# Optimization experiments

Hardware: AMD Instinct MI355X
Metric: run time of the kernel (lower is better)

The kernel has to match this reference:

```python
import math
import jax, jax.numpy as jnp
import numpy as np

B, N, C = 64, 1024, 128
RATIO = 0.5
EDGE_P = 0.02  # sparsity of the random binary adjacency


def setup_inputs() -> dict:
    key = jax.random.key(0)
    kx, ka, kw = jax.random.split(key, 3)
    x = jax.random.normal(kx, (B, N, C), dtype=jnp.float32)
    # binary adjacency (realistic graph input); module symmetrizes + clips anyway
    adj = (jax.random.uniform(ka, (B, N, N)) < EDGE_P).astype(jnp.float32)
    # TopKPooling learnable score weight (PyG initializes uniform; normal is fine for a baseline)
    w = jax.random.normal(kw, (C,), dtype=jnp.float32)
    return {"x": x, "adj": adj, "w": w}


def reference(x, adj, w):
    # x: [B, N, C], adj: [B, N, N], w: [C]
    b, n, c = x.shape
    k = int(math.ceil(RATIO * n))  # same k for every graph -> fully batched

    # per-sample: adj_tmp = adj + adj.T; adj_tmp[adj_tmp > 1] = 1
    a = adj + jnp.swapaxes(adj, 1, 2)
    a = jnp.minimum(a, 1.0)

    # TopKPooling score: tanh((x . w) / ||w||), select top-k nodes per graph
    score = jnp.tanh(jnp.einsum("bnc,c->bn", x, w) / jnp.linalg.norm(w))
    top_scores, perm = jax.lax.top_k(score, k)          # [B, k] each, descending

    # gated node features: x[perm] * score[perm]
    x_pool = jnp.take_along_axis(x, perm[..., None], axis=1) * top_scores[..., None]  # [B,k,C]

    # pooled dense adjacency: edges among selected nodes (to_dense_adj counts edges,
    # so entries are 1 where a nonzero edge existed) + 1 on diagonal from add_self_loops
    a_rows = jnp.take_along_axis(a, perm[:, :, None], axis=1)        # [B, k, N]
    a_sub = jnp.take_along_axis(a_rows, perm[:, None, :], axis=2)    # [B, k, k]
    adj_pooled = (a_sub != 0).astype(x.dtype) + jnp.eye(k, dtype=x.dtype)[None]

    return x_pool, adj_pooled
```

## Files before the change

kernel.cpp:

```cpp
#include <hip/hip_runtime.h>
#include <math.h>

#define NB 64
#define NN 1024
#define NC 128
#define NK 512

__global__ __launch_bounds__(1024) void score_kernel(
    const float* __restrict__ x, const float* __restrict__ w,
    double* __restrict__ sacc)
{
    const int i = blockIdx.x;
    const int b = i >> 3, oct = i & 7;
    const int t = threadIdx.x;
    const int c0 = (t & 15) * 8;
    const float4 wa = *(const float4*)(w + c0);
    const float4 wb = *(const float4*)(w + c0 + 4);
    #pragma unroll
    for (int pass = 0; pass < 2; ++pass) {
        int row = oct * 128 + pass * 64 + (t >> 4);
        const float* xr = x + ((size_t)b * NN + row) * NC + c0;
        float4 a  = *(const float4*)xr;
        float4 bb = *(const float4*)(xr + 4);
        double acc = (double)a.x * wa.x + (double)a.y * wa.y
                   + (double)a.z * wa.z + (double)a.w * wa.w
                   + (double)bb.x * wb.x + (double)bb.y * wb.y
                   + (double)bb.z * wb.z + (double)bb.w * wb.w;
        acc += __shfl_xor(acc, 1, 64);
        acc += __shfl_xor(acc, 2, 64);
        acc += __shfl_xor(acc, 4, 64);
        acc += __shfl_xor(acc, 8, 64);
        if ((t & 15) == 0) sacc[(size_t)b * NN + row] = acc;
    }
}

__global__ __launch_bounds__(1024) void rank_xpool_kernel(
    const double* __restrict__ sacc, const float* __restrict__ x,
    const float* __restrict__ w, int* __restrict__ perm,
    float* __restrict__ gate, int* __restrict__ inv,
    float* __restrict__ x_pool)
{
    __shared__ __align__(16) unsigned long long keys[NN];
    __shared__ int rp[1024];
    __shared__ double s_rnw;
    __shared__ int sel_nr[128];
    __shared__ float sel_g[128];
    __shared__ int scount;
    const int i = blockIdx.x;
    const int b = (i & 7) + ((i >> 6) << 3);
    const int h = (i >> 3) & 7;
    const int t = threadIdx.x;

    {
        double sv = sacc[(size_t)b * NN + t];
        long long bits = __double_as_longlong(sv);
        unsigned long long mono =
            (unsigned long long)(bits ^ ((bits >> 63) | 0x8000000000000000LL));
        keys[t] = (mono & ~1023ULL) | (unsigned long long)(1023 - t);
    }
    if (t < 64) {
        double p = (double)w[t] * (double)w[t]
                 + (double)w[t + 64] * (double)w[t + 64];
        #pragma unroll
        for (int off = 32; off > 0; off >>= 1)
            p += __shfl_xor(p, off, 64);
        if (t == 0) s_rnw = 1.0 / sqrt(p);
    }
    if (t == 0) scount = 0;
    __syncthreads();

    const int n  = h * 128 + (t & 127);
    const int jc = t >> 7;
    const unsigned long long mykey = keys[n];
    int r = 0;
    #pragma unroll 8
    for (int j2 = 0; j2 < 64; ++j2) {
        ulonglong2 kk = *(const ulonglong2*)&keys[jc * 128 + j2 * 2];
        r += (kk.x > mykey);
        r += (kk.y > mykey);
    }
    rp[t] = r;
    __syncthreads();
    if (t < 128) {
        int rr = 0;
        #pragma unroll
        for (int c = 0; c < 8; ++c) rr += rp[c * 128 + t];
        int n2 = h * 128 + t;
        inv[b * NN + n2] = (rr < NK) ? rr : -1;
        if (rr < NK) {
            double sv = sacc[(size_t)b * NN + n2];
            float gv = (float)tanh(sv * s_rnw);
            perm[b * NK + rr] = n2;
            gate[b * NK + rr] = gv;
            int slot = atomicAdd(&scount, 1);
            sel_nr[slot] = (n2 << 16) | rr;
            sel_g[slot]  = gv;
        }
    }
    __syncthreads();

    const int cnt = scount;
    const int rowSlot = t >> 5;
    const int lane = t & 31;
    for (int base = 0; base < cnt; base += 32) {
        int idx = base + rowSlot;
        if (idx < cnt) {
            int nr = sel_nr[idx];
            int n2 = nr >> 16, rr = nr & 0xffff;
            float g = sel_g[idx];
            float4 v = *(const float4*)(x + ((size_t)b * NN + n2) * NC + lane * 4);
            v.x *= g; v.y *= g; v.z *= g; v.w *= g;
            *(float4*)(x_pool + ((size_t)b * NK + rr) * NC + lane * 4) = v;
        }
    }
}

__global__ __launch_bounds__(1024) void adj_scan_kernel(
    const float* __restrict__ adj, const int* __restrict__ perm,
    const int* __restrict__ inv, unsigned* __restrict__ bm)
{
    __shared__ unsigned bits[64 * 17];
    __shared__ int sinv[NN];
    const int b = blockIdx.x >> 3;
    const int chunk = blockIdx.x & 7;
    const int t = threadIdx.x;
    for (int idx = t; idx < 64 * 17; idx += 1024) bits[idx] = 0;
    for (int idx = t; idx < NN; idx += 1024) sinv[idx] = inv[b * NN + idx];
    __syncthreads();

    const float* ab = adj + (size_t)b * NN * NN;
    const int* permb = perm + b * NK + chunk * 64;
    const int g  = t >> 8;
    const int lt = t & 255;

    int il = g;
    float4 v0 = *(const float4*)(ab + (size_t)permb[il]      * NN + lt * 4);
    float4 v1 = *(const float4*)(ab + (size_t)permb[il + 4]  * NN + lt * 4);
    float4 v2 = *(const float4*)(ab + (size_t)permb[il + 8]  * NN + lt * 4);
    float4 v3 = *(const float4*)(ab + (size_t)permb[il + 12] * NN + lt * 4);
    float4 v4 = *(const float4*)(ab + (size_t)permb[il + 16] * NN + lt * 4);
    float4 v5 = *(const float4*)(ab + (size_t)permb[il + 20] * NN + lt * 4);
    for (int it = 0; it < 16; ++it) {
        float4 vn = v0;
        if (it < 10)
            vn = *(const float4*)(ab + (size_t)permb[il + 24] * NN + lt * 4);
        #pragma unroll
        for (int u = 0; u < 4; ++u) {
            if (((const float*)&v0)[u] != 0.0f) {
                int j = sinv[lt * 4 + u];
                if (j >= 0)
                    atomicOr(&bits[il * 17 + (j >> 5)], 1u << (j & 31));
            }
        }
        v0 = v1; v1 = v2; v2 = v3; v3 = v4; v4 = v5; v5 = vn; il += 4;
    }
    __syncthreads();
    {
        int dil = t & 63, w = t >> 6;
        bm[(size_t)b * 8192 + w * 512 + chunk * 64 + dil] = bits[dil * 17 + w];
    }
}

__global__ __launch_bounds__(1024) void adj_write_kernel(
    const unsigned* __restrict__ bm, float* __restrict__ out)
{
    __shared__ unsigned tcb[2 * 512];
    __shared__ unsigned fws[64 * 17];
    const int b = blockIdx.x >> 3;
    const int slab = blockIdx.x & 7;
    const int t = threadIdx.x;
    const unsigned* bmb = bm + (size_t)b * 8192;
    if (t < 256) {
        *(uint4*)&tcb[t * 4] = *(const uint4*)&bmb[slab * 2 * 512 + t * 4];
    }
    {
        int il = t & 63, wi = t >> 6;
        fws[il * 17 + wi] = bmb[wi * 512 + slab * 64 + il];
    }
    __syncthreads();

    float* ob = out + ((size_t)b * NK + slab * 64) * NK;
    #pragma unroll
    for (int it = 0; it < 8; ++it) {
        int lid = it * 1024 + t;
        int i_loc = lid >> 7;
        int i = slab * 64 + i_loc;
        int j4 = (lid & 127) * 4;
        unsigned fw = fws[i_loc * 17 + (j4 >> 5)];
        uint4 tq = *(const uint4*)&tcb[(i_loc >> 5) * 512 + j4];
        float4 res;
        float* rpn = (float*)&res;
        const unsigned* tp = (const unsigned*)&tq;
        #pragma unroll
        for (int e = 0; e < 4; ++e) {
            unsigned bit = ((fw >> ((j4 + e) & 31)) | (tp[e] >> (i & 31))) & 1u;
            float f = (float)bit;
            if (i == j4 + e) f += 1.0f;
            rpn[e] = f;
        }
        *(float4*)(ob + (size_t)i_loc * NK + j4) = res;
    }
}

extern "C" void kernel_launch(void* const* d_in, const int* in_sizes, int n_in,
                              void* d_out, int out_size, void* d_ws, size_t ws_size,
                              hipStream_t stream) {
    const float* x   = (const float*)d_in[0];
    const float* adj = (const float*)d_in[1];
    const float* w   = (const float*)d_in[2];
    float* out = (float*)d_out;

    char* p = (char*)d_ws;
    double*   sacc = (double*)p;    p += sizeof(double) * NB * NN;
    unsigned* bm   = (unsigned*)p;  p += sizeof(unsigned) * NB * 16 * NK;
    int*      perm = (int*)p;       p += sizeof(int) * NB * NK;
    float*    gate = (float*)p;     p += sizeof(float) * NB * NK;
    int*      inv  = (int*)p;

    float* x_pool     = out;
    float* adj_pooled = out + (size_t)NB * NK * NC;

    score_kernel<<<NB * 8, 1024, 0, stream>>>(x, w, sacc);
    rank_xpool_kernel<<<NB * 8, 1024, 0, stream>>>(sacc, x, w, perm, gate, inv, x_pool);
    adj_scan_kernel<<<NB * 8, 1024, 0, stream>>>(adj, perm, inv, bm);
    adj_write_kernel<<<NB * 8, 1024, 0, stream>>>(bm, adj_pooled);
}
```

Baseline: 58.12 us.

## Fuse rank, adjacency scan and x_pool gather into one kernel with redundant ranking

Merges the rank/x_pool kernel and the adjacency-scan kernel into a single launch. Each block now recomputes the full 1024-node rank for its graph, so it can build the inverse map and its own 64-entry perm slice in shared memory rather than passing perm/gate/inv through global memory. Sort keys are now built in the score kernel, whose block-to-batch mapping is also changed. This removes one launch and the intermediate global round trips, but the O(N^2) rank comparison is now done 8 times per graph instead of once.

```diff
diff --git a/kernel.cpp b/kernel.cpp
--- a/kernel.cpp
+++ b/kernel.cpp
@@ -8,10 +8,11 @@
 
 __global__ __launch_bounds__(1024) void score_kernel(
     const float* __restrict__ x, const float* __restrict__ w,
-    double* __restrict__ sacc)
+    double* __restrict__ sacc, unsigned long long* __restrict__ keys_g)
 {
     const int i = blockIdx.x;
-    const int b = i >> 3, oct = i & 7;
+    const int b = (i & 7) + ((i >> 6) << 3);
+    const int oct = (i >> 3) & 7;
     const int t = threadIdx.x;
     const int c0 = (t & 15) * 8;
     const float4 wa = *(const float4*)(w + c0);
@@ -30,34 +31,37 @@
         acc += __shfl_xor(acc, 2, 64);
         acc += __shfl_xor(acc, 4, 64);
         acc += __shfl_xor(acc, 8, 64);
-        if ((t & 15) == 0) sacc[(size_t)b * NN + row] = acc;
-    }
-}
-
-__global__ __launch_bounds__(1024) void rank_xpool_kernel(
+        if ((t & 15) == 0) {
+            sacc[(size_t)b * NN + row] = acc;
+            long long sb = __double_as_longlong(acc);
+            unsigned long long mono =
+                (unsigned long long)(sb ^ ((sb >> 63) | 0x8000000000000000LL));
+            keys_g[(size_t)b * NN + row] =
+                (mono & ~1023ULL) | (unsigned long long)(1023 - row);
+        }
+    }
+}
+
+__global__ __launch_bounds__(1024) void rank_scan_xpool_kernel(
+    const unsigned long long* __restrict__ keys_g,
     const double* __restrict__ sacc, const float* __restrict__ x,
-    const float* __restrict__ w, int* __restrict__ perm,
-    float* __restrict__ gate, int* __restrict__ inv,
-    float* __restrict__ x_pool)
+    const float* __restrict__ w, const float* __restrict__ adj,
+    unsigned* __restrict__ bm, float* __restrict__ x_pool)
 {
     __shared__ __align__(16) unsigned long long keys[NN];
-    __shared__ int rp[1024];
+    __shared__ int sinv[NN];
+    __shared__ unsigned bits[64 * 17];
+    __shared__ int perm_l[64];
+    __shared__ float gate_l[64];
     __shared__ double s_rnw;
-    __shared__ int sel_nr[128];
-    __shared__ float sel_g[128];
-    __shared__ int scount;
     const int i = blockIdx.x;
     const int b = (i & 7) + ((i >> 6) << 3);
-    const int h = (i >> 3) & 7;
+    const int chunk = (i >> 3) & 7;
     const int t = threadIdx.x;
 
-    {
-        double sv = sacc[(size_t)b * NN + t];
-        long long bits = __double_as_longlong(sv);
-        unsigned long long mono =
-            (unsigned long long)(bits ^ ((bits >> 63) | 0x8000000000000000LL));
-        keys[t] = (mono & ~1023ULL) | (unsigned long long)(1023 - t);
-    }
+    for (int idx = t; idx < NN; idx += 1024)
+        keys[idx] = keys_g[(size_t)b * NN + idx];
+    for (int idx = t; idx < 64 * 17; idx += 1024) bits[idx] = 0;
     if (t < 64) {
         double p = (double)w[t] * (double)w[t]
                  + (double)w[t + 64] * (double)w[t + 64];
@@ -66,84 +70,40 @@
             p += __shfl_xor(p, off, 64);
         if (t == 0) s_rnw = 1.0 / sqrt(p);
     }
-    if (t == 0) scount = 0;
-    __syncthreads();
-
-    const int n  = h * 128 + (t & 127);
-    const int jc = t >> 7;
-    const unsigned long long mykey = keys[n];
-    int r = 0;
-    #pragma unroll 8
-    for (int j2 = 0; j2 < 64; ++j2) {
-        ulonglong2 kk = *(const ulonglong2*)&keys[jc * 128 + j2 * 2];
-        r += (kk.x > mykey);
-        r += (kk.y > mykey);
-    }
-    rp[t] = r;
-    __syncthreads();
-    if (t < 128) {
-        int rr = 0;
-        #pragma unroll
-        for (int c = 0; c < 8; ++c) rr += rp[c * 128 + t];
-        int n2 = h * 128 + t;
-        inv[b * NN + n2] = (rr < NK) ? rr : -1;
-        if (rr < NK) {
-            double sv = sacc[(size_t)b * NN + n2];
-            float gv = (float)tanh(sv * s_rnw);
-            perm[b * NK + rr] = n2;
-            gate[b * NK + rr] = gv;
-            int slot = atomicAdd(&scount, 1);
-            sel_nr[slot] = (n2 << 16) | rr;
-            sel_g[slot]  = gv;
-        }
-    }
-    __syncthreads();
-
-    const int cnt = scount;
-    const int rowSlot = t >> 5;
-    const int lane = t & 31;
-    for (int base = 0; base < cnt; base += 32) {
-        int idx = base + rowSlot;
-        if (idx < cnt) {
-            int nr = sel_nr[idx];
-            int n2 = nr >> 16, rr = nr & 0xffff;
-            float g = sel_g[idx];
-            float4 v = *(const float4*)(x + ((size_t)b * NN + n2) * NC + lane * 4);
-            v.x *= g; v.y *= g; v.z *= g; v.w *= g;
-            *(float4*)(x_pool + ((size_t)b * NK + rr) * NC + lane * 4) = v;
-        }
-    }
-}
-
-__global__ __launch_bounds__(1024) void adj_scan_kernel(
-    const float* __restrict__ adj, const int* __restrict__ perm,
-    const int* __restrict__ inv, unsigned* __restrict__ bm)
-{
-    __shared__ unsigned bits[64 * 17];
-    __shared__ int sinv[NN];
-    const int b = blockIdx.x >> 3;
-    const int chunk = blockIdx.x & 7;
-    const int t = threadIdx.x;
-    for (int idx = t; idx < 64 * 17; idx += 1024) bits[idx] = 0;
-    for (int idx = t; idx < NN; idx += 1024) sinv[idx] = inv[b * NN + idx];
+    __syncthreads();
+
+    {
+        const unsigned long long mykey = keys[t];
+        int r = 0;
+        #pragma unroll 8
+        for (int j = 0; j < NN; j += 2) {
+            ulonglong2 kk = *(const ulonglong2*)&keys[j];
+            r += (kk.x > mykey);
+            r += (kk.y > mykey);
+        }
+        sinv[t] = (r < NK) ? r : -1;
+        int rl = r - chunk * 64;
+        if (rl >= 0 && rl < 64) {
+            perm_l[rl] = t;
+            gate_l[rl] = (float)tanh(sacc[(size_t)b * NN + t] * s_rnw);
+        }
+    }
     __syncthreads();
 
     const float* ab = adj + (size_t)b * NN * NN;
-    const int* permb = perm + b * NK + chunk * 64;
     const int g  = t >> 8;
     const int lt = t & 255;
-
     int il = g;
-    float4 v0 = *(const float4*)(ab + (size_t)permb[il]      * NN + lt * 4);
-    float4 v1 = *(const float4*)(ab + (size_t)permb[il + 4]  * NN + lt * 4);
-    float4 v2 = *(const float4*)(ab + (size_t)permb[il + 8]  * NN + lt * 4);
-    float4 v3 = *(const float4*)(ab + (size_t)permb[il + 12] * NN + lt * 4);
-    float4 v4 = *(const float4*)(ab + (size_t)permb[il + 16] * NN + lt * 4);
-    float4 v5 = *(const float4*)(ab + (size_t)permb[il + 20] * NN + lt * 4);
+    float4 v0 = *(const float4*)(ab + (size_t)perm_l[il]      * NN + lt * 4);
+    float4 v1 = *(const float4*)(ab + (size_t)perm_l[il + 4]  * NN + lt * 4);
+    float4 v2 = *(const float4*)(ab + (size_t)perm_l[il + 8]  * NN + lt * 4);
+    float4 v3 = *(const float4*)(ab + (size_t)perm_l[il + 12] * NN + lt * 4);
+    float4 v4 = *(const float4*)(ab + (size_t)perm_l[il + 16] * NN + lt * 4);
+    float4 v5 = *(const float4*)(ab + (size_t)perm_l[il + 20] * NN + lt * 4);
     for (int it = 0; it < 16; ++it) {
         float4 vn = v0;
         if (it < 10)
-            vn = *(const float4*)(ab + (size_t)permb[il + 24] * NN + lt * 4);
+            vn = *(const float4*)(ab + (size_t)perm_l[il + 24] * NN + lt * 4);
         #pragma unroll
         for (int u = 0; u < 4; ++u) {
             if (((const float*)&v0)[u] != 0.0f) {
@@ -156,8 +116,21 @@
     }
     __syncthreads();
     {
-        int dil = t & 63, w = t >> 6;
-        bm[(size_t)b * 8192 + w * 512 + chunk * 64 + dil] = bits[dil * 17 + w];
+        int dil = t & 63, wd = t >> 6;
+        bm[(size_t)b * 8192 + wd * 512 + chunk * 64 + dil] = bits[dil * 17 + wd];
+    }
+
+    const int rowSlot = t >> 5;
+    const int lane = t & 31;
+    #pragma unroll
+    for (int base2 = 0; base2 < 64; base2 += 32) {
+        int il2 = base2 + rowSlot;
+        int n2 = perm_l[il2];
+        float gv = gate_l[il2];
+        int rr = chunk * 64 + il2;
+        float4 v = *(const float4*)(x + ((size_t)b * NN + n2) * NC + lane * 4);
+        v.x *= gv; v.y *= gv; v.z *= gv; v.w *= gv;
+        *(float4*)(x_pool + ((size_t)b * NK + rr) * NC + lane * 4) = v;
     }
 }
 
@@ -211,17 +184,17 @@
     float* out = (float*)d_out;
 
     char* p = (char*)d_ws;
-    double*   sacc = (double*)p;    p += sizeof(double) * NB * NN;
-    unsigned* bm   = (unsigned*)p;  p += sizeof(unsigned) * NB * 16 * NK;
-    int*      perm = (int*)p;       p += sizeof(int) * NB * NK;
-    float*    gate = (float*)p;     p += sizeof(float) * NB * NK;
-    int*      inv  = (int*)p;
+    double*             sacc   = (double*)p;
+    p += sizeof(double) * NB * NN;
+    unsigned long long* keys_g = (unsigned long long*)p;
+    p += sizeof(unsigned long long) * NB * NN;
+    unsigned*           bm     = (unsigned*)p;
 
     float* x_pool     = out;
     float* adj_pooled = out + (size_t)NB * NK * NC;
 
-    score_kernel<<<NB * 8, 1024, 0, stream>>>(x, w, sacc);
-    rank_xpool_kernel<<<NB * 8, 1024, 0, stream>>>(sacc, x, w, perm, gate, inv, x_pool);
-    adj_scan_kernel<<<NB * 8, 1024, 0, stream>>>(adj, perm, inv, bm);
+    score_kernel<<<NB * 8, 1024, 0, stream>>>(x, w, sacc, keys_g);
+    rank_scan_xpool_kernel<<<NB * 8, 1024, 0, stream>>>(
+        keys_g, sacc, x, w, adj, bm, x_pool);
     adj_write_kernel<<<NB * 8, 1024, 0, stream>>>(bm, adj_pooled);
 }
```

Result: slower. 77.46 us (+33.3%).
